# Performance work log

Hardware: AMD Instinct MI355X
Metric: run time of the kernel (lower is better)

Reference implementation:

```python
import jax, jax.numpy as jnp
import numpy as np

H = 16        # query heads
K = 4         # kv heads (GQA)
D = 128       # head_dim
HID = 2048    # hidden_size
T = 2048      # num tokens (single prefill sequence, causal)
THETA = 10000.0


def setup_inputs() -> dict:
    key = jax.random.key(0)
    k1, k2, k3 = jax.random.split(key, 3)
    hidden_states = jax.random.normal(k1, (T, HID), dtype=jnp.float32)
    position_ids = jnp.arange(T, dtype=jnp.int32)
    Wqkv = jax.random.normal(k2, (HID, (H + 2 * K) * D), dtype=jnp.float32) * 0.02
    Wo = jax.random.normal(k3, (H * D, HID), dtype=jnp.float32) * 0.02
    return {"hidden_states": hidden_states, "position_ids": position_ids,
            "Wqkv": Wqkv, "Wo": Wo}


def _rope_neox(x, pos):
    # x: [T, heads, D]; neox style: rotate halves
    half = D // 2
    inv_freq = 1.0 / (THETA ** (jnp.arange(0, D, 2, dtype=jnp.float32) / D))  # [D/2]
    ang = pos.astype(jnp.float32)[:, None] * inv_freq                          # [T, D/2]
    cos = jnp.cos(ang)[:, None, :]
    sin = jnp.sin(ang)[:, None, :]
    x1, x2 = x[..., :half], x[..., half:]
    return jnp.concatenate([x1 * cos - x2 * sin, x2 * cos + x1 * sin], axis=-1)


def reference(hidden_states, position_ids, Wqkv, Wo):
    t = hidden_states.shape[0]
    qkv = hidden_states @ Wqkv                                   # [T, (H+2K)*D]
    q = qkv[:, : H * D].reshape(t, H, D)
    k = qkv[:, H * D : (H + K) * D].reshape(t, K, D)
    v = qkv[:, (H + K) * D :].reshape(t, K, D)
    q = _rope_neox(q, position_ids)
    k = _rope_neox(k, position_ids)
    # GQA: expand kv heads to H
    rep = H // K
    k = jnp.repeat(k, rep, axis=1)                               # [T, H, D]
    v = jnp.repeat(v, rep, axis=1)
    scale = D ** -0.5
    scores = jnp.einsum('qhd,khd->hqk', q, k) * scale            # [H, T, T]
    causal = jnp.arange(t)[:, None] >= jnp.arange(t)[None, :]    # [T, T]
    scores = jnp.where(causal[None], scores, jnp.finfo(scores.dtype).min)
    probs = jax.nn.softmax(scores, axis=-1)
    ctx = jnp.einsum('hqk,khd->qhd', probs, v).reshape(t, H * D)  # [T, H*D]
    return ctx @ Wo                                              # [T, HID]
```

## Files before the change

kernel.cpp:

```cpp
#include <hip/hip_runtime.h>
#include <hip/hip_bf16.h>
#include <stdint.h>

typedef __hip_bfloat16 bf16;
typedef __attribute__((ext_vector_type(8))) short bh8;
typedef __attribute__((ext_vector_type(4))) float f32x4;

#define MFMA16(a, b, c) __builtin_amdgcn_mfma_f32_16x16x32_bf16((a), (b), (c), 0, 0, 0)

typedef const __attribute__((address_space(1))) void* gas1_t;
typedef __attribute__((address_space(3))) void* las3_t;

__device__ __forceinline__ void gload_lds16(const void* g, void* l) {
  __builtin_amdgcn_global_load_lds((gas1_t)g, (las3_t)l, 16, 0, 0);
}

__device__ __forceinline__ float bfu2f(unsigned short u) {
  union { unsigned int i; float f; } c;
  c.i = (unsigned int)u << 16;
  return c.f;
}

__global__ __launch_bounds__(256) void cast_f32_bf16(const float* __restrict__ x,
                                                     bf16* __restrict__ y, int n4) {
  int i = blockIdx.x * 256 + threadIdx.x;
  if (i >= n4) return;
  float4 v = ((const float4*)x)[i];
  union { ushort4 u; bf16 b[4]; } o;
  o.b[0] = __float2bfloat16(v.x);
  o.b[1] = __float2bfloat16(v.y);
  o.b[2] = __float2bfloat16(v.z);
  o.b[3] = __float2bfloat16(v.w);
  ((ushort4*)y)[i] = o.u;
}

__global__ __launch_bounds__(256) void transpose_cast(const float* __restrict__ W,
                                                      bf16* __restrict__ WT, int R, int C) {
  __shared__ float tile[32][33];
  const int tx = threadIdx.x & 31, ty = threadIdx.x >> 5;
  const int bx = blockIdx.x, by = blockIdx.y;
#pragma unroll
  for (int p = 0; p < 4; ++p)
    tile[ty + p * 8][tx] = W[(long)(by * 32 + ty + p * 8) * C + bx * 32 + tx];
  __syncthreads();
#pragma unroll
  for (int p = 0; p < 4; ++p)
    WT[(long)(bx * 32 + ty + p * 8) * R + by * 32 + tx] = __float2bfloat16(tile[tx][ty + p * 8]);
}

template <bool BF16OUT>
__global__ __launch_bounds__(256) void gemm_bt_sk(const bf16* __restrict__ A,
                                                  const bf16* __restrict__ BT,
                                                  void* __restrict__ C0, void* __restrict__ C1,
                                                  int M, int N, int Kd, int nKs) {
  __shared__ bf16 As[128 * 64];
  __shared__ bf16 Bs[128 * 64];
  const int tid = threadIdx.x, lane = tid & 63, wid = tid >> 6;
  const int wr = wid >> 1, wc = wid & 1;
  const int bx = blockIdx.x, by = blockIdx.y, z = blockIdx.z;

  f32x4 acc[4][4];
#pragma unroll
  for (int m = 0; m < 4; ++m)
#pragma unroll
    for (int n = 0; n < 4; ++n)
#pragma unroll
      for (int r = 0; r < 4; ++r) acc[m][n][r] = 0.0f;

  const long Abase = (long)(by * 128) * Kd;
  const long Bbase = (long)(bx * 128) * Kd;
  const int lr = lane & 15, lh = lane >> 4;
  const int k00 = z * nKs * 64;

  for (int kt = 0; kt < nKs; ++kt) {
    __syncthreads();
    const int k0 = k00 + kt * 64;
#pragma unroll
    for (int i = 0; i < 4; ++i) {
      const int cb = i * 256 + wid * 64;
      const int c = cb + lane;
      const int row = c >> 3, s = c & 7;
      gload_lds16(A + Abase + (long)row * Kd + k0 + (s ^ (row & 7)) * 8, (char*)As + cb * 16);
      gload_lds16(BT + Bbase + (long)row * Kd + k0 + (s ^ (row & 7)) * 8, (char*)Bs + cb * 16);
    }
    __syncthreads();

#pragma unroll
    for (int kk = 0; kk < 2; ++kk) {
      bh8 af[4], bfv[4];
#pragma unroll
      for (int m = 0; m < 4; ++m)
        af[m] = *(const bh8*)((const char*)As +
                              (((wr * 64 + m * 16 + lr) * 128 + kk * 64 + lh * 16) ^
                               ((lr & 7) << 4)));
#pragma unroll
      for (int n = 0; n < 4; ++n)
        bfv[n] = *(const bh8*)((const char*)Bs +
                               (((wc * 64 + n * 16 + lr) * 128 + kk * 64 + lh * 16) ^
                                ((lr & 7) << 4)));
#pragma unroll
      for (int m = 0; m < 4; ++m)
#pragma unroll
        for (int n = 0; n < 4; ++n) acc[m][n] = MFMA16(af[m], bfv[n], acc[m][n]);
    }
  }

  const int r0 = by * 128 + wr * 64, c0 = bx * 128 + wc * 64;
  const int lrow = lh * 4;
  if (BF16OUT) {
    bf16* P = (bf16*)(z == 0 ? C0 : C1);
#pragma unroll
    for (int m = 0; m < 4; ++m)
#pragma unroll
      for (int n = 0; n < 4; ++n)
#pragma unroll
        for (int r = 0; r < 4; ++r)
          P[(long)(r0 + m * 16 + lrow + r) * N + c0 + n * 16 + lr] =
              __float2bfloat16(acc[m][n][r]);
  } else {
    float* P = (float*)(z == 0 ? C0 : C1);
#pragma unroll
    for (int m = 0; m < 4; ++m)
#pragma unroll
      for (int n = 0; n < 4; ++n)
#pragma unroll
        for (int r = 0; r < 4; ++r)
          P[(long)(r0 + m * 16 + lrow + r) * N + c0 + n * 16 + lr] = acc[m][n][r];
  }
}

__global__ __launch_bounds__(256) void out_reduce(float* __restrict__ out,
                                                  const float* __restrict__ p1, int n4) {
  int i = blockIdx.x * 256 + threadIdx.x;
  if (i >= n4) return;
  float4 a = ((const float4*)out)[i];
  float4 b = ((const float4*)p1)[i];
  a.x += b.x; a.y += b.y; a.z += b.z; a.w += b.w;
  ((float4*)out)[i] = a;
}

__global__ __launch_bounds__(256) void rope_split(const bf16* __restrict__ P0,
                                                  const bf16* __restrict__ P1,
                                                  const int* __restrict__ pos_ids,
                                                  bf16* __restrict__ Qb, bf16* __restrict__ Kb,
                                                  bf16* __restrict__ VbT) {
  const int t = blockIdx.x;
  const int tid = threadIdx.x;
  const float pos = (float)pos_ids[t];
  const ushort* r0 = (const ushort*)(P0 + (long)t * 3072);
  const ushort* r1 = (const ushort*)(P1 + (long)t * 3072);
  for (int i = tid; i < 512; i += 256) {
    const int kvh = i >> 7, d = i & 127;
    const float v = bfu2f(r0[2560 + i]) + bfu2f(r1[2560 + i]);
    VbT[(long)(kvh * 128 + d) * 2048 + t] = __float2bfloat16(v);
  }
  for (int i = tid; i < 1280; i += 256) {
    const int hh = i >> 6, d = i & 63;
    const float inv = exp2f((float)d * -0.2076205059304594f);
    const float ang = pos * inv;
    const float c = cosf(ang), s = sinf(ang);
    const float x1 = bfu2f(r0[hh * 128 + d]) + bfu2f(r1[hh * 128 + d]);
    const float x2 = bfu2f(r0[hh * 128 + d + 64]) + bfu2f(r1[hh * 128 + d + 64]);
    const float o1 = x1 * c - x2 * s, o2 = x2 * c + x1 * s;
    if (hh < 16) {
      Qb[(long)t * 2048 + hh * 128 + d] = __float2bfloat16(o1);
      Qb[(long)t * 2048 + hh * 128 + d + 64] = __float2bfloat16(o2);
    } else {
      Kb[t * 512 + (hh - 16) * 128 + d] = __float2bfloat16(o1);
      Kb[t * 512 + (hh - 16) * 128 + d + 64] = __float2bfloat16(o2);
    }
  }
}

__global__ __launch_bounds__(256) void attn_partial(const bf16* __restrict__ Qb,
                                                    const bf16* __restrict__ Kb,
                                                    const bf16* __restrict__ VbT,
                                                    bf16* __restrict__ Pctx,
                                                    float* __restrict__ ML) {
  const int h = blockIdx.x;
  const int qb = 31 - blockIdx.y;
  const int z = blockIdx.z;
  const int kh = h >> 2;
  const int tid = threadIdx.x, lane = tid & 63, w = tid >> 6;
  const int pid = (h * 32 + qb) * 2 + z;

  const int nt = qb + 1;
  const int half = (nt + 1) >> 1;
  const int kt0 = z * half;
  const int kt1 = (z == 0) ? half : nt;

  if (kt0 >= kt1) {
    if (tid < 64) {
      ML[pid * 128 + tid] = -1e30f;
      ML[pid * 128 + 64 + tid] = 0.0f;
    }
    ushort4 z4 = make_ushort4(0, 0, 0, 0);
    ushort4* pz = (ushort4*)(Pctx + (long)pid * 8192);
    for (int j = tid; j < 2048; j += 256) pz[j] = z4;
    return;
  }

  __shared__ bf16 Kl[64 * 128];
  __shared__ bf16 Vt[128 * 64];
  __shared__ bf16 Pl[4][16 * 72];

  const int lr = lane & 15, lh = lane >> 4;
  const int q0w = qb * 64 + w * 16;

  bh8 qf[4];
#pragma unroll
  for (int dc = 0; dc < 4; ++dc)
    qf[dc] = *(const bh8*)&Qb[(long)(q0w + lr) * 2048 + h * 128 + dc * 32 + lh * 8];

  f32x4 ctx[8];
#pragma unroll
  for (int i = 0; i < 8; ++i)
#pragma unroll
    for (int r = 0; r < 4; ++r) ctx[i][r] = 0.0f;
  float mrun[4], lrun[4];
#pragma unroll
  for (int r = 0; r < 4; ++r) { mrun[r] = -1e30f; lrun[r] = 0.0f; }

  const float scale = 0.08838834764831845f;

  for (int kt = kt0; kt < kt1; ++kt) {
    __syncthreads();
    const long Kbase = ((long)(kt * 64) * 4 + kh) * 128;
#pragma unroll
    for (int i = 0; i < 4; ++i) {
      const int cb = i * 256 + w * 64;
      const int c = cb + lane;
      const int krow = c >> 4, s = c & 15;
      gload_lds16(Kb + Kbase + (long)krow * 512 + (s ^ (krow & 7)) * 8, (char*)Kl + cb * 16);
    }
    const long Vbase = (long)kh * 128 * 2048 + kt * 64;
#pragma unroll
    for (int i = 0; i < 4; ++i) {
      const int cb = i * 256 + w * 64;
      const int c = cb + lane;
      const int vrow = c >> 3, s = c & 7;
      gload_lds16(VbT + Vbase + (long)vrow * 2048 + (s ^ (vrow & 7)) * 8, (char*)Vt + cb * 16);
    }
    __syncthreads();

    f32x4 S[4];
#pragma unroll
    for (int kb = 0; kb < 4; ++kb) {
#pragma unroll
      for (int r = 0; r < 4; ++r) S[kb][r] = 0.0f;
#pragma unroll
      for (int dc = 0; dc < 4; ++dc) {
        const int key = kb * 16 + lr;
        const int byteoff = (key * 256 + dc * 64 + lh * 16) ^ ((lr & 7) << 4);
        bh8 kf = *(const bh8*)((const char*)Kl + byteoff);
        S[kb] = MFMA16(qf[dc], kf, S[kb]);
      }
    }

    float sv[4][4], tmax[4];
#pragma unroll
    for (int r = 0; r < 4; ++r) tmax[r] = -1e30f;
    if (kt == qb) {
#pragma unroll
      for (int kb = 0; kb < 4; ++kb)
#pragma unroll
        for (int r = 0; r < 4; ++r) {
          float s = S[kb][r] * scale;
          const int kg = kt * 64 + kb * 16 + lr;
          const int qg = q0w + lh * 4 + r;
          if (kg > qg) s = -1e30f;
          sv[kb][r] = s;
          tmax[r] = fmaxf(tmax[r], s);
        }
    } else {
#pragma unroll
      for (int kb = 0; kb < 4; ++kb)
#pragma unroll
        for (int r = 0; r < 4; ++r) {
          float s = S[kb][r] * scale;
          sv[kb][r] = s;
          tmax[r] = fmaxf(tmax[r], s);
        }
    }
#pragma unroll
    for (int r = 0; r < 4; ++r) {
#pragma unroll
      for (int x = 1; x < 16; x <<= 1) tmax[r] = fmaxf(tmax[r], __shfl_xor(tmax[r], x, 64));
    }
    float alpha[4];
#pragma unroll
    for (int r = 0; r < 4; ++r) {
      const float mnew = fmaxf(mrun[r], tmax[r]);
      alpha[r] = __expf(mrun[r] - mnew);
      mrun[r] = mnew;
      lrun[r] *= alpha[r];
    }
#pragma unroll
    for (int kb = 0; kb < 4; ++kb)
#pragma unroll
      for (int r = 0; r < 4; ++r) {
        const float p = __expf(sv[kb][r] - mrun[r]);
        lrun[r] += p;
        Pl[w][(lh * 4 + r) * 72 + kb * 16 + lr] = __float2bfloat16(p);
      }
#pragma unroll
    for (int i = 0; i < 8; ++i)
#pragma unroll
      for (int r = 0; r < 4; ++r) ctx[i][r] *= alpha[r];
#pragma unroll
    for (int kc = 0; kc < 2; ++kc) {
      bh8 pa = *(const bh8*)&Pl[w][lr * 72 + kc * 32 + lh * 8];
#pragma unroll
      for (int dblk = 0; dblk < 8; ++dblk) {
        const int vrow = dblk * 16 + lr;
        const int voff = (vrow * 128 + kc * 64 + lh * 16) ^ ((lr & 7) << 4);
        bh8 vb = *(const bh8*)((const char*)Vt + voff);
        ctx[dblk] = MFMA16(pa, vb, ctx[dblk]);
      }
    }
  }

  float lsum[4];
#pragma unroll
  for (int r = 0; r < 4; ++r) {
    float l = lrun[r];
#pragma unroll
    for (int x = 1; x < 16; x <<= 1) l += __shfl_xor(l, x, 64);
    lsum[r] = l;
  }
  if (lr == 0) {
#pragma unroll
    for (int r = 0; r < 4; ++r) {
      ML[pid * 128 + w * 16 + lh * 4 + r] = mrun[r];
      ML[pid * 128 + 64 + w * 16 + lh * 4 + r] = lsum[r];
    }
  }
#pragma unroll
  for (int dblk = 0; dblk < 8; ++dblk)
#pragma unroll
    for (int r = 0; r < 4; ++r)
      Pctx[(long)pid * 8192 + (w * 16 + lh * 4 + r) * 128 + dblk * 16 + lr] =
          __float2bfloat16(ctx[dblk][r]);
}

__global__ __launch_bounds__(256) void attn_merge(const bf16* __restrict__ Pctx,
                                                  const float* __restrict__ ML,
                                                  bf16* __restrict__ out) {
  const int h = blockIdx.x, qb = blockIdx.y;
  const int tid = threadIdx.x;
  const int r = tid >> 2, seg = tid & 3;
  const int pid0 = (h * 32 + qb) * 2;
  const float m0 = ML[pid0 * 128 + r], l0 = ML[pid0 * 128 + 64 + r];
  const float m1 = ML[pid0 * 128 + 128 + r], l1 = ML[pid0 * 128 + 192 + r];
  const float m = fmaxf(m0, m1);
  float a0 = __expf(m0 - m), a1 = __expf(m1 - m);
  const float inv = 1.0f / (l0 * a0 + l1 * a1);
  a0 *= inv;
  a1 *= inv;
  const ushort* p0 = (const ushort*)(Pctx + (long)pid0 * 8192 + r * 128 + seg * 32);
  const ushort* p1 = p0 + 8192;
  bf16* o = out + (long)(qb * 64 + r) * 2048 + h * 128 + seg * 32;
#pragma unroll
  for (int j = 0; j < 4; ++j) {
    union { bh8 v; ushort s[8]; } v0, v1;
    v0.v = *(const bh8*)(p0 + j * 8);
    v1.v = *(const bh8*)(p1 + j * 8);
    union { ushort4 u; bf16 b[4]; } o0, o1;
#pragma unroll
    for (int e = 0; e < 4; ++e) {
      o0.b[e] = __float2bfloat16(bfu2f(v0.s[e]) * a0 + bfu2f(v1.s[e]) * a1);
      o1.b[e] = __float2bfloat16(bfu2f(v0.s[e + 4]) * a0 + bfu2f(v1.s[e + 4]) * a1);
    }
    *(ushort4*)(o + j * 8) = o0.u;
    *(ushort4*)(o + j * 8 + 4) = o1.u;
  }
}

extern "C" void kernel_launch(void* const* d_in, const int* in_sizes, int n_in,
                              void* d_out, int out_size, void* d_ws, size_t ws_size,
                              hipStream_t stream) {
  const float* hs = (const float*)d_in[0];
  const int* pos = (const int*)d_in[1];
  const float* Wqkv = (const float*)d_in[2];
  const float* Wo = (const float*)d_in[3];
  char* ws = (char*)d_ws;

  bf16* hsb = (bf16*)(ws);
  bf16* ctx = (bf16*)(ws);
  bf16* wqkvT = (bf16*)(ws + (8l << 20));
  bf16* Qb = (bf16*)(ws + (8l << 20));
  bf16* Kb = (bf16*)(ws + (16l << 20));
  bf16* VbT = (bf16*)(ws + (18l << 20));
  bf16* woT = (bf16*)(ws + (20l << 20));
  bf16* qkvP0 = (bf16*)(ws + (28l << 20));
  bf16* qkvP1 = (bf16*)(ws + (40l << 20));
  bf16* Pctx = (bf16*)(ws + (28l << 20));
  float* ML = (float*)(ws + (44l << 20));
  float* outP1 = (float*)(ws + (28l << 20));

  cast_f32_bf16<<<4096, 256, 0, stream>>>(hs, hsb, 2048 * 2048 / 4);
  transpose_cast<<<dim3(3072 / 32, 2048 / 32), 256, 0, stream>>>(Wqkv, wqkvT, 2048, 3072);
  transpose_cast<<<dim3(2048 / 32, 2048 / 32), 256, 0, stream>>>(Wo, woT, 2048, 2048);
  gemm_bt_sk<true><<<dim3(24, 16, 2), 256, 0, stream>>>(hsb, wqkvT, qkvP0, qkvP1,
                                                        2048, 3072, 2048, 16);
  rope_split<<<2048, 256, 0, stream>>>(qkvP0, qkvP1, pos, Qb, Kb, VbT);
  attn_partial<<<dim3(16, 32, 2), 256, 0, stream>>>(Qb, Kb, VbT, Pctx, ML);
  attn_merge<<<dim3(16, 32), 256, 0, stream>>>(Pctx, ML, ctx);
  gemm_bt_sk<false><<<dim3(16, 16, 2), 256, 0, stream>>>(ctx, woT, d_out, outP1,
                                                         2048, 2048, 2048, 16);
  out_reduce<<<4096, 256, 0, stream>>>((float*)d_out, outP1, 2048 * 2048 / 4);
}
```

Before: 234.7 us.

## Compute transposed S so P feeds PV MFMA from registers, add lazy rescale

Computes S^T (keys x queries) by swapping the MFMA operands and permuting key rows, so each lane's softmax probabilities already sit in the A-operand layout for the PV MFMA. This removes the LDS round trip for P and most of the cross-lane max/sum shuffles. It also folds the softmax scale into Q during rope, skips the ctx rescale unless the running max rises by more than a threshold, changes the K swizzle and adds an occupancy hint to launch_bounds. The lazy rescale keeps unnormalised values slightly larger and the fold changes bf16 rounding of Q a little.

```diff
diff --git a/kernel.cpp b/kernel.cpp
--- a/kernel.cpp
+++ b/kernel.cpp
@@ -147,6 +147,7 @@
   const int t = blockIdx.x;
   const int tid = threadIdx.x;
   const float pos = (float)pos_ids[t];
+  const float qscale = 0.08838834764831845f;
   const ushort* r0 = (const ushort*)(P0 + (long)t * 3072);
   const ushort* r1 = (const ushort*)(P1 + (long)t * 3072);
   for (int i = tid; i < 512; i += 256) {
@@ -163,8 +164,8 @@
     const float x2 = bfu2f(r0[hh * 128 + d + 64]) + bfu2f(r1[hh * 128 + d + 64]);
     const float o1 = x1 * c - x2 * s, o2 = x2 * c + x1 * s;
     if (hh < 16) {
-      Qb[(long)t * 2048 + hh * 128 + d] = __float2bfloat16(o1);
-      Qb[(long)t * 2048 + hh * 128 + d + 64] = __float2bfloat16(o2);
+      Qb[(long)t * 2048 + hh * 128 + d] = __float2bfloat16(o1 * qscale);
+      Qb[(long)t * 2048 + hh * 128 + d + 64] = __float2bfloat16(o2 * qscale);
     } else {
       Kb[t * 512 + (hh - 16) * 128 + d] = __float2bfloat16(o1);
       Kb[t * 512 + (hh - 16) * 128 + d + 64] = __float2bfloat16(o2);
@@ -172,11 +173,11 @@
   }
 }
 
-__global__ __launch_bounds__(256) void attn_partial(const bf16* __restrict__ Qb,
-                                                    const bf16* __restrict__ Kb,
-                                                    const bf16* __restrict__ VbT,
-                                                    bf16* __restrict__ Pctx,
-                                                    float* __restrict__ ML) {
+__global__ __launch_bounds__(256, 4) void attn_partial(const bf16* __restrict__ Qb,
+                                                       const bf16* __restrict__ Kb,
+                                                       const bf16* __restrict__ VbT,
+                                                       bf16* __restrict__ Pctx,
+                                                       float* __restrict__ ML) {
   const int h = blockIdx.x;
   const int qb = 31 - blockIdx.y;
   const int z = blockIdx.z;
@@ -202,7 +203,6 @@
 
   __shared__ bf16 Kl[64 * 128];
   __shared__ bf16 Vt[128 * 64];
-  __shared__ bf16 Pl[4][16 * 72];
 
   const int lr = lane & 15, lh = lane >> 4;
   const int q0w = qb * 64 + w * 16;
@@ -217,11 +217,7 @@
   for (int i = 0; i < 8; ++i)
 #pragma unroll
     for (int r = 0; r < 4; ++r) ctx[i][r] = 0.0f;
-  float mrun[4], lrun[4];
-#pragma unroll
-  for (int r = 0; r < 4; ++r) { mrun[r] = -1e30f; lrun[r] = 0.0f; }
-
-  const float scale = 0.08838834764831845f;
+  float mrun = -1e30f, lrun = 0.0f;
 
   for (int kt = kt0; kt < kt1; ++kt) {
     __syncthreads();
@@ -231,7 +227,8 @@
       const int cb = i * 256 + w * 64;
       const int c = cb + lane;
       const int krow = c >> 4, s = c & 15;
-      gload_lds16(Kb + Kbase + (long)krow * 512 + (s ^ (krow & 7)) * 8, (char*)Kl + cb * 16);
+      const int g = s ^ ((krow & 3) | ((krow & 8) >> 1));
+      gload_lds16(Kb + Kbase + (long)krow * 512 + g * 8, (char*)Kl + cb * 16);
     }
     const long Vbase = (long)kh * 128 * 2048 + kt * 64;
 #pragma unroll
@@ -243,97 +240,91 @@
     }
     __syncthreads();
 
-    f32x4 S[4];
-#pragma unroll
-    for (int kb = 0; kb < 4; ++kb) {
-#pragma unroll
-      for (int r = 0; r < 4; ++r) S[kb][r] = 0.0f;
-#pragma unroll
-      for (int dc = 0; dc < 4; ++dc) {
-        const int key = kb * 16 + lr;
-        const int byteoff = (key * 256 + dc * 64 + lh * 16) ^ ((lr & 7) << 4);
-        bh8 kf = *(const bh8*)((const char*)Kl + byteoff);
-        S[kb] = MFMA16(qf[dc], kf, S[kb]);
+    f32x4 S[2][2];
+#pragma unroll
+    for (int kc = 0; kc < 2; ++kc)
+#pragma unroll
+      for (int b = 0; b < 2; ++b) {
+#pragma unroll
+        for (int r = 0; r < 4; ++r) S[kc][b][r] = 0.0f;
+        const int key = kc * 32 + ((lr >> 2) << 3) + b * 4 + (lr & 3);
+        const int kbase = key * 256 + lh * 16;
+#pragma unroll
+        for (int dc = 0; dc < 4; ++dc) {
+          bh8 kf = *(const bh8*)((const char*)Kl + ((kbase + dc * 64) ^ ((lr & 7) << 4)));
+          S[kc][b] = MFMA16(kf, qf[dc], S[kc][b]);
+        }
       }
-    }
-
-    float sv[4][4], tmax[4];
-#pragma unroll
-    for (int r = 0; r < 4; ++r) tmax[r] = -1e30f;
+
     if (kt == qb) {
-#pragma unroll
-      for (int kb = 0; kb < 4; ++kb)
+      const int qg = q0w + lr;
+#pragma unroll
+      for (int kc = 0; kc < 2; ++kc)
+#pragma unroll
+        for (int b = 0; b < 2; ++b)
+#pragma unroll
+          for (int r = 0; r < 4; ++r) {
+            const int kg = kt * 64 + kc * 32 + lh * 8 + b * 4 + r;
+            if (kg > qg) S[kc][b][r] = -1e30f;
+          }
+    }
+
+    float pm = -1e30f;
+#pragma unroll
+    for (int kc = 0; kc < 2; ++kc)
+#pragma unroll
+      for (int b = 0; b < 2; ++b)
+#pragma unroll
+        for (int r = 0; r < 4; ++r) pm = fmaxf(pm, S[kc][b][r]);
+    pm = fmaxf(pm, __shfl_xor(pm, 16, 64));
+    pm = fmaxf(pm, __shfl_xor(pm, 32, 64));
+
+    if (__any(pm > mrun + 4.0f)) {
+      const float mnew = fmaxf(mrun, pm);
+      const float alpha = __expf(mrun - mnew);
+      mrun = mnew;
+      lrun *= alpha;
+      float a4[4];
+#pragma unroll
+      for (int r = 0; r < 4; ++r) a4[r] = __shfl(alpha, lh * 4 + r, 64);
+#pragma unroll
+      for (int i = 0; i < 8; ++i)
+#pragma unroll
+        for (int r = 0; r < 4; ++r) ctx[i][r] *= a4[r];
+    }
+
+    bh8 pa[2];
+#pragma unroll
+    for (int kc = 0; kc < 2; ++kc) {
+      union { bh8 v; bf16 e[8]; } pk;
+#pragma unroll
+      for (int b = 0; b < 2; ++b)
 #pragma unroll
         for (int r = 0; r < 4; ++r) {
-          float s = S[kb][r] * scale;
-          const int kg = kt * 64 + kb * 16 + lr;
-          const int qg = q0w + lh * 4 + r;
-          if (kg > qg) s = -1e30f;
-          sv[kb][r] = s;
-          tmax[r] = fmaxf(tmax[r], s);
+          const float p = __expf(S[kc][b][r] - mrun);
+          lrun += p;
+          pk.e[b * 4 + r] = __float2bfloat16(p);
         }
-    } else {
-#pragma unroll
-      for (int kb = 0; kb < 4; ++kb)
-#pragma unroll
-        for (int r = 0; r < 4; ++r) {
-          float s = S[kb][r] * scale;
-          sv[kb][r] = s;
-          tmax[r] = fmaxf(tmax[r], s);
-        }
-    }
-#pragma unroll
-    for (int r = 0; r < 4; ++r) {
-#pragma unroll
-      for (int x = 1; x < 16; x <<= 1) tmax[r] = fmaxf(tmax[r], __shfl_xor(tmax[r], x, 64));
-    }
-    float alpha[4];
-#pragma unroll
-    for (int r = 0; r < 4; ++r) {
-      const float mnew = fmaxf(mrun[r], tmax[r]);
-      alpha[r] = __expf(mrun[r] - mnew);
-      mrun[r] = mnew;
-      lrun[r] *= alpha[r];
-    }
-#pragma unroll
-    for (int kb = 0; kb < 4; ++kb)
-#pragma unroll
-      for (int r = 0; r < 4; ++r) {
-        const float p = __expf(sv[kb][r] - mrun[r]);
-        lrun[r] += p;
-        Pl[w][(lh * 4 + r) * 72 + kb * 16 + lr] = __float2bfloat16(p);
-      }
-#pragma unroll
-    for (int i = 0; i < 8; ++i)
-#pragma unroll
-      for (int r = 0; r < 4; ++r) ctx[i][r] *= alpha[r];
-#pragma unroll
-    for (int kc = 0; kc < 2; ++kc) {
-      bh8 pa = *(const bh8*)&Pl[w][lr * 72 + kc * 32 + lh * 8];
+      pa[kc] = pk.v;
+    }
+
+#pragma unroll
+    for (int kc = 0; kc < 2; ++kc)
 #pragma unroll
       for (int dblk = 0; dblk < 8; ++dblk) {
         const int vrow = dblk * 16 + lr;
         const int voff = (vrow * 128 + kc * 64 + lh * 16) ^ ((lr & 7) << 4);
         bh8 vb = *(const bh8*)((const char*)Vt + voff);
-        ctx[dblk] = MFMA16(pa, vb, ctx[dblk]);
+        ctx[dblk] = MFMA16(pa[kc], vb, ctx[dblk]);
       }
-    }
-  }
-
-  float lsum[4];
-#pragma unroll
-  for (int r = 0; r < 4; ++r) {
-    float l = lrun[r];
-#pragma unroll
-    for (int x = 1; x < 16; x <<= 1) l += __shfl_xor(l, x, 64);
-    lsum[r] = l;
-  }
-  if (lr == 0) {
-#pragma unroll
-    for (int r = 0; r < 4; ++r) {
-      ML[pid * 128 + w * 16 + lh * 4 + r] = mrun[r];
-      ML[pid * 128 + 64 + w * 16 + lh * 4 + r] = lsum[r];
-    }
+  }
+
+  float l = lrun;
+  l += __shfl_xor(l, 16, 64);
+  l += __shfl_xor(l, 32, 64);
+  if (lh == 0) {
+    ML[pid * 128 + w * 16 + lr] = mrun;
+    ML[pid * 128 + 64 + w * 16 + lr] = l;
   }
 #pragma unroll
   for (int dblk = 0; dblk < 8; ++dblk)
```

Result: slower. 244.4 us (+4.1%).
